# Kernel tuning notes

Measured on AMD Instinct MI355X. Metric: run time of the kernel, lower is better.

Reference implementation:

```python
import jax, jax.numpy as jnp
import numpy as np

B, D, K, BETA = 32, 64, 1024, 0.25


def _conv(x, w, b, s=1, p=0):
    y = jax.lax.conv_general_dilated(x, w, (s, s), [(p, p), (p, p)],
                                     dimension_numbers=('NCHW', 'OIHW', 'NCHW'))
    return y + b[None, :, None, None]


def _tconv(x, w, b):
    # PyTorch ConvTranspose2d(k=4, s=2, p=1); w layout (C_in, C_out, 4, 4)
    wt = jnp.flip(w, (2, 3)).transpose(1, 0, 2, 3)
    y = jax.lax.conv_general_dilated(x, wt, (1, 1), [(2, 2), (2, 2)],
                                     lhs_dilation=(2, 2),
                                     dimension_numbers=('NCHW', 'OIHW', 'NCHW'))
    return y + b[None, :, None, None]


def _res(x, w1, b1, w2, b2):
    # Residual: x + conv1x1(relu(conv3x3(relu(x))))  (no BN config)
    h = _conv(jax.nn.relu(x), w1, b1, 1, 1)
    h = _conv(jax.nn.relu(h), w2, b2, 1, 0)
    return x + h


def setup_inputs() -> dict:
    ks = iter(jax.random.split(jax.random.key(0), 64))

    def w(*shape):
        fan = int(np.prod(shape[1:]))
        return (jax.random.normal(next(ks), shape, jnp.float32) / np.sqrt(fan)).astype(jnp.float32)

    def z(n):
        return jnp.zeros((n,), jnp.float32)

    inp = dict(
        x=jax.random.normal(next(ks), (B, 3, 256, 256), jnp.float32),
        enc_w0=w(64, 3, 4, 4), enc_b0=z(64),
        enc_w1=w(128, 64, 4, 4), enc_b1=z(128),
        enc_w2=w(256, 128, 4, 4), enc_b2=z(256),
        enc_r0_w1=w(64, 256, 3, 3), enc_r0_b1=z(64),
        enc_r0_w2=w(256, 64, 1, 1), enc_r0_b2=z(256),
        enc_r1_w1=w(64, 256, 3, 3), enc_r1_b1=z(64),
        enc_r1_w2=w(256, 64, 1, 1), enc_r1_b2=z(256),
        enc_adj_w=w(D, 256, 1, 1), enc_adj_b=z(D),
        codebook=(jax.random.normal(next(ks), (K, D), jnp.float32) / np.sqrt(D)).astype(jnp.float32),
        dec_adj_w=w(256, D, 1, 1), dec_adj_b=z(256),
        dec_r0_w1=w(64, 256, 3, 3), dec_r0_b1=z(64),
        dec_r0_w2=w(256, 64, 1, 1), dec_r0_b2=z(256),
        dec_r1_w1=w(64, 256, 3, 3), dec_r1_b1=z(64),
        dec_r1_w2=w(256, 64, 1, 1), dec_r1_b2=z(256),
        dec_tw0=w(256, 128, 4, 4), dec_tb0=z(128),
        dec_tw1=w(128, 64, 4, 4), dec_tb1=z(64),
        dec_tw2=w(64, 32, 4, 4), dec_tb2=z(32),
        out_w=w(3, 32, 1, 1), out_b=z(3),
    )
    return inp


def reference(x, enc_w0, enc_b0, enc_w1, enc_b1, enc_w2, enc_b2,
              enc_r0_w1, enc_r0_b1, enc_r0_w2, enc_r0_b2,
              enc_r1_w1, enc_r1_b1, enc_r1_w2, enc_r1_b2,
              enc_adj_w, enc_adj_b, codebook, dec_adj_w, dec_adj_b,
              dec_r0_w1, dec_r0_b1, dec_r0_w2, dec_r0_b2,
              dec_r1_w1, dec_r1_b1, dec_r1_w2, dec_r1_b2,
              dec_tw0, dec_tb0, dec_tw1, dec_tb1, dec_tw2, dec_tb2,
              out_w, out_b):
    # ---------- encoder (M=7: three stride-2 convs, no BN) ----------
    h = jax.nn.relu(_conv(x, enc_w0, enc_b0, 2, 1))   # [B,64,128,128]
    h = jax.nn.relu(_conv(h, enc_w1, enc_b1, 2, 1))   # [B,128,64,64]
    h = jax.nn.relu(_conv(h, enc_w2, enc_b2, 2, 1))   # [B,256,32,32]
    h = _res(h, enc_r0_w1, enc_r0_b1, enc_r0_w2, enc_r0_b2)
    h = _res(h, enc_r1_w1, enc_r1_b1, enc_r1_w2, enc_r1_b2)
    zlat = _conv(h, enc_adj_w, enc_adj_b)             # [B,D,32,32]
    # ---------- vector quantization ----------
    zp = zlat.transpose(0, 2, 3, 1)                   # [B,32,32,D]
    zf = zp.reshape(-1, D)                            # [N,D], N = B*32*32
    d = (jnp.sum(zf * zf, 1, keepdims=True)
         - 2.0 * (zf @ codebook.T)
         + jnp.sum(codebook * codebook, 1)[None, :])  # [N,K]
    idx = jnp.argmin(d, axis=1)                       # [N] codebook indices
    q = codebook[idx].reshape(zp.shape)
    sg = jax.lax.stop_gradient
    e_loss = jnp.mean((sg(q) - zp) ** 2)              # commitment
    q_loss = jnp.mean((q - sg(zp)) ** 2)              # codebook
    vq_loss = q_loss + BETA * e_loss
    q_st = zp + sg(q - zp)                            # straight-through
    counts = jnp.zeros((K,), jnp.float32).at[idx].add(1.0)
    probs = counts / zf.shape[0]
    perplexity = jnp.exp(-jnp.sum(probs * jnp.log(probs + 1e-10)))
    hq = q_st.transpose(0, 3, 1, 2)                   # [B,D,32,32]
    # ---------- decoder (M=7: three stride-2 transposed convs) ----------
    h = _conv(hq, dec_adj_w, dec_adj_b)               # [B,256,32,32]
    h = _res(h, dec_r0_w1, dec_r0_b1, dec_r0_w2, dec_r0_b2)
    h = _res(h, dec_r1_w1, dec_r1_b1, dec_r1_w2, dec_r1_b2)
    h = jax.nn.relu(_tconv(h, dec_tw0, dec_tb0))      # [B,128,64,64]
    h = jax.nn.relu(_tconv(h, dec_tw1, dec_tb1))      # [B,64,128,128]
    h = jax.nn.relu(_tconv(h, dec_tw2, dec_tb2))      # [B,32,256,256]
    x_recon = _conv(h, out_w, out_b)                  # [B,3,256,256]
    return x_recon, vq_loss, perplexity
```

## Files before the change

kernel.cpp:

```cpp
#include <hip/hip_runtime.h>
#include <math.h>

typedef __attribute__((ext_vector_type(4))) float f32x4;
typedef __attribute__((ext_vector_type(8))) short short8;
typedef __attribute__((ext_vector_type(4))) unsigned int u32x4;
typedef unsigned short ushort_t;
typedef unsigned int uint_t;

static const size_t A_OFF      = 0;
static const size_t C_OFF      = 0;
static const size_t D_OFF      = 9469952;
static const size_t E_OFF      = 18939904;
static const size_t Q_OFF      = 21037056;
static const size_t B_OFF      = 34611200;
static const size_t CBT_OFF    = 52453376;
static const size_t CNORM_OFF  = 52518912;
static const size_t COUNTS_OFF = 52519936;
static const size_t SUMSQ_OFF  = 52520960;
static const size_t WT_OFF     = 52520964;

__device__ __forceinline__ ushort_t f2b(float f) {
  uint_t u = __float_as_uint(f);
  uint_t r = (u + 0x7FFFu + ((u >> 16) & 1u)) >> 16;
  return (ushort_t)r;
}
__device__ __forceinline__ float b2f(ushort_t h) {
  return __uint_as_float(((uint_t)h) << 16);
}

__global__ void k_halo(float* __restrict__ buf, int HP, int WP) {
  const int plane = blockIdx.x;
  float* p = buf + (size_t)plane * HP * WP;
  const int ring = 2 * (HP + WP) - 4;
  for (int i = threadIdx.x; i < ring; i += blockDim.x) {
    int idx;
    if (i < WP) idx = i;
    else if (i < 2 * WP) idx = (HP - 1) * WP + (i - WP);
    else {
      const int j = i - 2 * WP;
      const int r = 1 + (j >> 1);
      idx = r * WP + ((j & 1) ? (WP - 1) : 0);
    }
    p[idx] = 0.0f;
  }
}
__global__ void k_zero(float* __restrict__ counts, float* __restrict__ sumsq) {
  const int t = blockIdx.x * 256 + threadIdx.x;
  if (t < 1024) counts[t] = 0.0f;
  if (t == 0) sumsq[0] = 0.0f;
}

__device__ __forceinline__ void wt_conv_body(const float* w, float* wT,
                                             int Cin, int Cout, int K) {
  const int n = Cin * Cout * K;
  for (int i = blockIdx.x * 256 + threadIdx.x; i < n; i += gridDim.x * 256) {
    const int co = i % Cout;
    const int k  = (i / Cout) % K;
    const int ci = i / (Cout * K);
    wT[i] = w[((size_t)co * Cin + ci) * K + k];
  }
}
__global__ void k_wt_conv_multi(const float* w0, float* o0, const float* w1, float* o1,
                                const float* w2, float* o2) {
  if (blockIdx.y == 0) wt_conv_body(w0, o0, 3, 64, 16);
  else if (blockIdx.y == 1) wt_conv_body(w1, o1, 256, 64, 1);
  else wt_conv_body(w2, o2, 64, 256, 1);
}
__device__ __forceinline__ void wtb_body(const float* w, ushort_t* wbT,
                                         int Cin, int Cout) {
  const int n = 4 * Cout * Cin * 4;
  for (int i = blockIdx.x * 256 + threadIdx.x; i < n; i += gridDim.x * 256) {
    const int tap = i & 3;
    const int ci  = (i >> 2) % Cin;
    const int co  = ((i >> 2) / Cin) % Cout;
    const int ph  = (i >> 2) / (Cin * Cout);
    const int ey = ph >> 1, ex = ph & 1;
    const int ty = tap >> 1, tx = tap & 1;
    const int kidx = (3 - 2 * ty - ey) * 4 + (3 - 2 * tx - ex);
    wbT[i] = f2b(w[((size_t)ci * Cout + co) * 16 + kidx]);
  }
}
__global__ void k_wtb_multi(const float* t0, ushort_t* o0, const float* t1, ushort_t* o1,
                            const float* t2, ushort_t* o2) {
  if (blockIdx.y == 0) wtb_body(t0, o0, 256, 128);
  else if (blockIdx.y == 1) wtb_body(t1, o1, 128, 64);
  else wtb_body(t2, o2, 64, 32);
}
__device__ __forceinline__ void wsplit_body(const float* w, ushort_t* wh,
                                            ushort_t* wl, int n) {
  for (int i = blockIdx.x * 256 + threadIdx.x; i < n; i += gridDim.x * 256) {
    const float v = w[i];
    const ushort_t h = f2b(v);
    wh[i] = h;
    wl[i] = f2b(v - b2f(h));
  }
}
__global__ void k_wsplit_enc(const float* w1, ushort_t* h1, ushort_t* l1,
                             const float* w2, ushort_t* h2, ushort_t* l2) {
  if (blockIdx.y == 0) wsplit_body(w1, h1, l1, 131072);
  else wsplit_body(w2, h2, l2, 524288);
}
__global__ void k_wsplit_w2m(const float* a, ushort_t* ah, ushort_t* al,
                             const float* b, ushort_t* bh, ushort_t* bl,
                             const float* c, ushort_t* ch, ushort_t* cl,
                             const float* d, ushort_t* dh, ushort_t* dl) {
  if (blockIdx.y == 0) wsplit_body(a, ah, al, 16384);
  else if (blockIdx.y == 1) wsplit_body(b, bh, bl, 16384);
  else if (blockIdx.y == 2) wsplit_body(c, ch, cl, 16384);
  else wsplit_body(d, dh, dl, 16384);
}
__device__ __forceinline__ void wt3_body(const float* w, ushort_t* wh, ushort_t* wl) {
  const int n = 9 * 64 * 256;
  for (int i = blockIdx.x * 256 + threadIdx.x; i < n; i += gridDim.x * 256) {
    const int ci = i & 255;
    const int co = (i >> 8) & 63;
    const int t  = i >> 14;
    const float v = w[((size_t)co * 256 + ci) * 9 + t];
    const ushort_t h = f2b(v);
    wh[i] = h;
    wl[i] = f2b(v - b2f(h));
  }
}
__global__ void k_wt3split_multi(const float* a, ushort_t* ah, ushort_t* al,
                                 const float* b, ushort_t* bh, ushort_t* bl,
                                 const float* c, ushort_t* ch, ushort_t* cl,
                                 const float* d, ushort_t* dh, ushort_t* dl) {
  if (blockIdx.y == 0) wt3_body(a, ah, al);
  else if (blockIdx.y == 1) wt3_body(b, bh, bl);
  else if (blockIdx.y == 2) wt3_body(c, ch, cl);
  else wt3_body(d, dh, dl);
}
__global__ void k_cbt(const float* __restrict__ cb, float* __restrict__ cbT,
                      float* __restrict__ cnorm) {
  const int c = blockIdx.x * 256 + threadIdx.x;
  float s = 0.0f;
  for (int ci = 0; ci < 64; ++ci) {
    const float v = cb[(size_t)c * 64 + ci];
    s += v * v;
    cbT[(size_t)ci * 1024 + c] = v;
  }
  cnorm[c] = s;
}

__global__ __launch_bounds__(256) void k_conv4s2_s3(
    const float* __restrict__ in, const float* __restrict__ wT,
    const float* __restrict__ bias, float* __restrict__ out) {
  const int b   = blockIdx.z;
  const int co0 = blockIdx.y << 4;
  const int oy0 = (blockIdx.x >> 2) << 5;
  const int ox0 = (blockIdx.x & 3) << 5;
  const int tid = threadIdx.x;
  const int ty = tid >> 4, tx = tid & 15;
  __shared__ float tin[3][66][67];
  float acc[4][16];
#pragma unroll
  for (int p = 0; p < 4; ++p)
#pragma unroll
    for (int co = 0; co < 16; ++co) acc[p][co] = 0.0f;

  const int iy0 = (oy0 << 1) - 1, ix0 = (ox0 << 1) - 1;
  for (int c = 0; c < 3; ++c) {
    const float* ip = in + (size_t)(b * 3 + c) * 65536;
    for (int j = tid; j < 66 * 66; j += 256) {
      const int r = j / 66, col = j - r * 66;
      const int iy = iy0 + r, ix = ix0 + col;
      float v = 0.0f;
      if ((unsigned)iy < 256u && (unsigned)ix < 256u) v = ip[iy * 256 + ix];
      tin[c][r][col] = v;
    }
  }
  __syncthreads();
#pragma unroll
  for (int c = 0; c < 3; ++c) {
    const float* wp = wT + (size_t)c * 16 * 64 + co0;
#pragma unroll
    for (int ky = 0; ky < 4; ++ky)
#pragma unroll
      for (int kx = 0; kx < 4; ++kx) {
        const float v0 = tin[c][2 * ty + ky][2 * tx + kx];
        const float v1 = tin[c][2 * ty + ky][2 * tx + 32 + kx];
        const float v2 = tin[c][2 * ty + 32 + ky][2 * tx + kx];
        const float v3 = tin[c][2 * ty + 32 + ky][2 * tx + 32 + kx];
        const float* wk = wp + (ky * 4 + kx) * 64;
#pragma unroll
        for (int co = 0; co < 16; ++co) {
          const float wv = wk[co];
          acc[0][co] = fmaf(v0, wv, acc[0][co]);
          acc[1][co] = fmaf(v1, wv, acc[1][co]);
          acc[2][co] = fmaf(v2, wv, acc[2][co]);
          acc[3][co] = fmaf(v3, wv, acc[3][co]);
        }
      }
  }
#pragma unroll
  for (int co = 0; co < 16; ++co) {
    const float bv = bias[co0 + co];
    float* op = out + (size_t)(b * 64 + co0 + co) * 16900;
    op[(size_t)(oy0 + ty + 1) * 130 + ox0 + tx + 1]        = fmaxf(acc[0][co] + bv, 0.0f);
    op[(size_t)(oy0 + ty + 1) * 130 + ox0 + tx + 17]       = fmaxf(acc[1][co] + bv, 0.0f);
    op[(size_t)(oy0 + ty + 17) * 130 + ox0 + tx + 1]       = fmaxf(acc[2][co] + bv, 0.0f);
    op[(size_t)(oy0 + ty + 17) * 130 + ox0 + tx + 17]      = fmaxf(acc[3][co] + bv, 0.0f);
  }
}

template <int WSHIFT, int CIN, int COUT, int WP, int INSTRIDE, int WOP, int OUTSTRIDE>
__global__ __launch_bounds__(256) void k_conv4s2_mfma(
    const float* __restrict__ in, const ushort_t* __restrict__ wbh,
    const ushort_t* __restrict__ wbl, const float* __restrict__ bias,
    float* __restrict__ out) {
  constexpr int W = 1 << WSHIFT;
  constexpr int NCH = CIN / 2;
  __shared__ __align__(16) short lsAh[64 * 40];
  __shared__ __align__(16) short lsAl[64 * 40];
  __shared__ __align__(16) short lsBh[64 * 40];
  __shared__ __align__(16) short lsBl[64 * 40];

  const int tid = threadIdx.x;
  const int b = blockIdx.z;
  const int co_b0 = blockIdx.y << 6;
  const int pxb0 = blockIdx.x << 6;

  const int spx = tid & 63;
  const int kg  = tid >> 6;
  const int sy = (pxb0 + spx) >> WSHIFT;
  const int sx = (pxb0 + spx) & (W - 1);
  const float* ipa = in + (size_t)(b * CIN + (kg >> 1)) * INSTRIDE
                   + (size_t)(2 * sy + 2 * (kg & 1)) * WP + 2 * sx;
  const ushort_t* wbase_h = wbh + (size_t)(co_b0 + spx) * (CIN * 16) + kg * 8;
  const ushort_t* wbase_l = wbl + (size_t)(co_b0 + spx) * (CIN * 16) + kg * 8;

  const int lane = tid & 63, wid = tid >> 6;
  const int wm = wid & 1, wn = wid >> 1;
  const int arow = lane & 15, ag = lane >> 4;

  f32x4 acc[2][2];
#pragma unroll
  for (int m = 0; m < 2; ++m)
#pragma unroll
    for (int n = 0; n < 2; ++n) acc[m][n] = (f32x4){0.f, 0.f, 0.f, 0.f};

  float pa[8];
  u32x4 pbh, pbl;
  auto loadch = [&](int ch) {
    const float* p = ipa + (size_t)ch * 2 * INSTRIDE;
    pa[0] = p[0];  pa[1] = p[1];      pa[2] = p[2];      pa[3] = p[3];
    pa[4] = p[WP]; pa[5] = p[WP + 1]; pa[6] = p[WP + 2]; pa[7] = p[WP + 3];
    pbh = *(const u32x4*)(wbase_h + (size_t)ch * 32);
    pbl = *(const u32x4*)(wbase_l + (size_t)ch * 32);
  };

  loadch(0);
  for (int ch = 0; ch < NCH; ++ch) {
    __syncthreads();
    u32x4 vh, vl;
#pragma unroll
    for (int j = 0; j < 4; ++j) {
      const ushort_t h0 = f2b(pa[2 * j]);
      const ushort_t h1 = f2b(pa[2 * j + 1]);
      const ushort_t l0 = f2b(pa[2 * j] - b2f(h0));
      const ushort_t l1 = f2b(pa[2 * j + 1] - b2f(h1));
      vh[j] = (uint_t)h0 | ((uint_t)h1 << 16);
      vl[j] = (uint_t)l0 | ((uint_t)l1 << 16);
    }
    *(u32x4*)(&lsAh[spx * 40 + kg * 8]) = vh;
    *(u32x4*)(&lsAl[spx * 40 + kg * 8]) = vl;
    *(u32x4*)(&lsBh[spx * 40 + kg * 8]) = pbh;
    *(u32x4*)(&lsBl[spx * 40 + kg * 8]) = pbl;
    if (ch + 1 < NCH) loadch(ch + 1);
    __syncthreads();
    short8 ah[2], al[2], bh[2], bl[2];
#pragma unroll
    for (int m = 0; m < 2; ++m) {
      ah[m] = *(const short8*)(&lsAh[(wm * 32 + m * 16 + arow) * 40 + ag * 8]);
      al[m] = *(const short8*)(&lsAl[(wm * 32 + m * 16 + arow) * 40 + ag * 8]);
    }
#pragma unroll
    for (int n = 0; n < 2; ++n) {
      bh[n] = *(const short8*)(&lsBh[(wn * 32 + n * 16 + arow) * 40 + ag * 8]);
      bl[n] = *(const short8*)(&lsBl[(wn * 32 + n * 16 + arow) * 40 + ag * 8]);
    }
#pragma unroll
    for (int m = 0; m < 2; ++m)
#pragma unroll
      for (int n = 0; n < 2; ++n) {
        acc[m][n] = __builtin_amdgcn_mfma_f32_16x16x32_bf16(ah[m], bh[n], acc[m][n], 0, 0, 0);
        acc[m][n] = __builtin_amdgcn_mfma_f32_16x16x32_bf16(ah[m], bl[n], acc[m][n], 0, 0, 0);
        acc[m][n] = __builtin_amdgcn_mfma_f32_16x16x32_bf16(al[m], bh[n], acc[m][n], 0, 0, 0);
      }
  }

#pragma unroll
  for (int m = 0; m < 2; ++m)
#pragma unroll
    for (int n = 0; n < 2; ++n) {
      const int col = co_b0 + wn * 32 + n * 16 + arow;
      const float bv = bias[col];
      float* obase = out + (size_t)(b * COUT + col) * OUTSTRIDE;
#pragma unroll
      for (int r = 0; r < 4; ++r) {
        const int pxl = pxb0 + wm * 32 + m * 16 + ag * 4 + r;
        const int yy = pxl >> WSHIFT, xx = pxl & (W - 1);
        obase[(size_t)(yy + 1) * WOP + (xx + 1)] = fmaxf(acc[m][n][r] + bv, 0.0f);
      }
    }
}

__global__ __launch_bounds__(512) void k_res_mfma(
    const float* __restrict__ in, const ushort_t* __restrict__ w3h,
    const ushort_t* __restrict__ w3l, const float* __restrict__ b1,
    const ushort_t* __restrict__ w2h, const ushort_t* __restrict__ w2l,
    const float* __restrict__ b2, float* __restrict__ out) {
  __shared__ __align__(16) short smem[10240];
  short* lsAh = smem;
  short* lsAl = smem + 2560;
  short* lsBh = smem + 5120;
  short* lsBl = smem + 7680;

  const int tid = threadIdx.x;
  const int b = blockIdx.z;
  const int pxb0 = blockIdx.x << 6;
  const bool isA = tid < 256;
  const int sidx = tid & 63;
  const int skg  = (tid >> 6) & 3;

  const int py = (pxb0 + sidx) >> 5;
  const int pxx = (pxb0 + sidx) & 31;
  const float* ipa = in + (size_t)b * 256 * 1156 + (size_t)py * 34 + pxx;

  const int lane = tid & 63, wid = tid >> 6;
  const int wm = wid & 1, wn = wid >> 1;
  const int arow = lane & 15, ag = lane >> 4;

  f32x4 acc[2];
  acc[0] = (f32x4){0.f, 0.f, 0.f, 0.f};
  acc[1] = (f32x4){0.f, 0.f, 0.f, 0.f};

  float pa[8];
  u32x4 pbh, pbl;
  auto loadit = [&](int it) {
    const int t = it >> 3, ck = it & 7;
    if (isA) {
      const int dy = t / 3, dx = t - 3 * (t / 3);
      const float* p = ipa + (size_t)(ck * 32 + skg * 8) * 1156 + dy * 34 + dx;
#pragma unroll
      for (int j = 0; j < 8; ++j) pa[j] = p[(size_t)j * 1156];
    } else {
      const ushort_t* ph = w3h + ((size_t)(t * 64 + sidx) << 8) + ck * 32 + skg * 8;
      const ushort_t* pl = w3l + ((size_t)(t * 64 + sidx) << 8) + ck * 32 + skg * 8;
      pbh = *(const u32x4*)ph;
      pbl = *(const u32x4*)pl;
    }
  };

  loadit(0);
  for (int it = 0; it < 72; ++it) {
    __syncthreads();
    if (isA) {
      u32x4 vh, vl;
#pragma unroll
      for (int j = 0; j < 4; ++j) {
        const float v0 = fmaxf(pa[2 * j], 0.0f);
        const float v1 = fmaxf(pa[2 * j + 1], 0.0f);
        const ushort_t h0 = f2b(v0);
        const ushort_t h1 = f2b(v1);
        const ushort_t l0 = f2b(v0 - b2f(h0));
        const ushort_t l1 = f2b(v1 - b2f(h1));
        vh[j] = (uint_t)h0 | ((uint_t)h1 << 16);
        vl[j] = (uint_t)l0 | ((uint_t)l1 << 16);
      }
      *(u32x4*)(&lsAh[sidx * 40 + skg * 8]) = vh;
      *(u32x4*)(&lsAl[sidx * 40 + skg * 8]) = vl;
    } else {
      *(u32x4*)(&lsBh[sidx * 40 + skg * 8]) = pbh;
      *(u32x4*)(&lsBl[sidx * 40 + skg * 8]) = pbl;
    }
    if (it + 1 < 72) loadit(it + 1);
    __syncthreads();
    short8 ah[2], al[2];
#pragma unroll
    for (int m = 0; m < 2; ++m) {
      ah[m] = *(const short8*)(&lsAh[(wm * 32 + m * 16 + arow) * 40 + ag * 8]);
      al[m] = *(const short8*)(&lsAl[(wm * 32 + m * 16 + arow) * 40 + ag * 8]);
    }
    const short8 bh = *(const short8*)(&lsBh[(wn * 16 + arow) * 40 + ag * 8]);
    const short8 bl = *(const short8*)(&lsBl[(wn * 16 + arow) * 40 + ag * 8]);
#pragma unroll
    for (int m = 0; m < 2; ++m) {
      acc[m] = __builtin_amdgcn_mfma_f32_16x16x32_bf16(ah[m], bh, acc[m], 0, 0, 0);
      acc[m] = __builtin_amdgcn_mfma_f32_16x16x32_bf16(ah[m], bl, acc[m], 0, 0, 0);
      acc[m] = __builtin_amdgcn_mfma_f32_16x16x32_bf16(al[m], bh, acc[m], 0, 0, 0);
    }
  }

  __syncthreads();
  {
    const float bv = b1[wn * 16 + arow];
    short* hh = smem;
    short* hl = smem + 4608;
#pragma unroll
    for (int m = 0; m < 2; ++m)
#pragma unroll
      for (int r = 0; r < 4; ++r) {
        const int pxl = wm * 32 + m * 16 + ag * 4 + r;
        const float v = fmaxf(acc[m][r] + bv, 0.0f);
        const ushort_t h = f2b(v);
        hh[pxl * 72 + wn * 16 + arow] = (short)h;
        hl[pxl * 72 + wn * 16 + arow] = (short)f2b(v - b2f(h));
      }
  }
  __syncthreads();

  const int m2 = wid & 3;
  const int nh = wid >> 2;
  const short* hh = smem;
  const short* hl = smem + 4608;
  short8 a2h[2], a2l[2];
#pragma unroll
  for (int c = 0; c < 2; ++c) {
    a2h[c] = *(const short8*)(&hh[(m2 * 16 + arow) * 72 + c * 32 + ag * 8]);
    a2l[c] = *(const short8*)(&hl[(m2 * 16 + arow) * 72 + c * 32 + ag * 8]);
  }
  const int px0 = pxb0 + m2 * 16 + ag * 4;
  const int yy0 = px0 >> 5, xx0 = px0 & 31;
  const int ridx = (yy0 + 1) * 34 + xx0 + 1;

  short8 cbh[2], cbl[2], nbh[2], nbl[2];
  float rv[4], nrv[4], bvc, nbvc;
  auto loadj = [&](int j, short8* oh, short8* ol, float* rr, float* bb) {
    const int col2 = (nh * 8 + j) * 16 + arow;
#pragma unroll
    for (int c = 0; c < 2; ++c) {
      oh[c] = *(const short8*)(w2h + (size_t)col2 * 64 + c * 32 + ag * 8);
      ol[c] = *(const short8*)(w2l + (size_t)col2 * 64 + c * 32 + ag * 8);
    }
    const float* rbase = in + (size_t)(b * 256 + col2) * 1156 + ridx;
#pragma unroll
    for (int r = 0; r < 4; ++r) rr[r] = rbase[r];
    *bb = b2[col2];
  };

  loadj(0, cbh, cbl, rv, &bvc);
#pragma unroll
  for (int j = 0; j < 8; ++j) {
    if (j + 1 < 8) loadj(j + 1, nbh, nbl, nrv, &nbvc);
    f32x4 acc2 = (f32x4){0.f, 0.f, 0.f, 0.f};
#pragma unroll
    for (int c = 0; c < 2; ++c) {
      acc2 = __builtin_amdgcn_mfma_f32_16x16x32_bf16(a2h[c], cbh[c], acc2, 0, 0, 0);
      acc2 = __builtin_amdgcn_mfma_f32_16x16x32_bf16(a2h[c], cbl[c], acc2, 0, 0, 0);
      acc2 = __builtin_amdgcn_mfma_f32_16x16x32_bf16(a2l[c], cbh[c], acc2, 0, 0, 0);
    }
    const int col2 = (nh * 8 + j) * 16 + arow;
    float* obase = out + (size_t)(b * 256 + col2) * 1156 + ridx;
#pragma unroll
    for (int r = 0; r < 4; ++r) obase[r] = acc2[r] + bvc + rv[r];
#pragma unroll
    for (int c = 0; c < 2; ++c) { cbh[c] = nbh[c]; cbl[c] = nbl[c]; }
#pragma unroll
    for (int r = 0; r < 4; ++r) rv[r] = nrv[r];
    bvc = nbvc;
  }
}

template <int IN_RELU, int HAS_RES, int IN_PAD, int OUT_PAD>
__global__ __launch_bounds__(256) void k_conv1x1_px(
    const float* __restrict__ in, const float* __restrict__ wT,
    const float* __restrict__ bias, const float* __restrict__ res,
    float* __restrict__ out, int Cin, int Cout) {
  const int b   = blockIdx.z;
  const int co0 = blockIdx.y << 4;
  const int px  = blockIdx.x * 256 + threadIdx.x;
  const int ppad = 35 + px + 2 * (px >> 5);
  const int ioff = IN_PAD ? ppad : px;
  const int istr = IN_PAD ? 1156 : 1024;
  const int ooff = OUT_PAD ? ppad : px;
  const int ostr = OUT_PAD ? 1156 : 1024;
  float acc[16];
#pragma unroll
  for (int co = 0; co < 16; ++co) acc[co] = 0.0f;
  const float* ip = in + (size_t)b * Cin * istr + ioff;
  const float* wp = wT + co0;
  for (int ci = 0; ci < Cin; ++ci) {
    float v = *ip;
    if (IN_RELU) v = fmaxf(v, 0.0f);
    ip += istr;
#pragma unroll
    for (int co = 0; co < 16; ++co) acc[co] = fmaf(v, wp[co], acc[co]);
    wp += Cout;
  }
  float* op = out + (size_t)(b * Cout + co0) * ostr + ooff;
  const float* rp = res + (size_t)(b * Cout + co0) * ostr + ooff;
#pragma unroll
  for (int co = 0; co < 16; ++co) {
    float r = acc[co] + bias[co0 + co];
    if (HAS_RES) r += rp[(size_t)co * ostr];
    op[(size_t)co * ostr] = r;
  }
}

template <int PXB, int COB, int WSHIFT, int CIN, int COUT, int WP,
          int INSTRIDE, int WOP, int OUTSTRIDE, int FINAL, int GRP>
__global__ __launch_bounds__(256) void k_tconv_mfma(
    const float* __restrict__ in, const ushort_t* __restrict__ wbT,
    const float* __restrict__ bias, const float* __restrict__ ow,
    const float* __restrict__ ob, float* __restrict__ out) {
  constexpr int W = 1 << WSHIFT;
  constexpr int NCH = CIN / 8;
  constexpr int NGRP = NCH / GRP;
  constexpr int PXSH = (PXB == 64) ? 6 : 7;
  constexpr int COSH = (COB == 64) ? 6 : 5;
  constexpr int NKG = (PXB * 4) / 256;
  constexpr int KGSTEP = 256 / PXB;
  __shared__ __align__(16) short lsA[GRP][PXB * 40];
  __shared__ __align__(16) short lsB[GRP][COB * 40];
  __shared__ float pxco[FINAL ? PXB : 1][33];

  const int tid = threadIdx.x;
  const int b = blockIdx.z;
  const int phase = blockIdx.y & 3;
  const int ey = phase >> 1, ex = phase & 1;
  const int co_b0 = (blockIdx.y >> 2) * COB;
  const int pxb0 = blockIdx.x * PXB;

  const int spx = tid & (PXB - 1);
  const int kg0 = tid >> PXSH;
  const int sy = (pxb0 + spx) >> WSHIFT;
  const int sx = (pxb0 + spx) & (W - 1);
  const float* ipa = in + (size_t)b * CIN * INSTRIDE + (size_t)(sy + ey) * WP + (sx + ex);
  const int sco = tid & (COB - 1);
  const int skg = tid >> COSH;
  const bool bstage = (tid < COB * 4);
  const ushort_t* wrow = wbT + ((size_t)(phase * COUT + co_b0 + sco) * CIN) * 4;

  const int lane = tid & 63, wid = tid >> 6;
  const int wm = wid % (PXB / 32), wn = wid / (PXB / 32);
  const int arow = lane & 15, ag = lane >> 4;

  f32x4 acc[2][2];
#pragma unroll
  for (int m = 0; m < 2; ++m)
#pragma unroll
    for (int n = 0; n < 2; ++n) acc[m][n] = (f32x4){0.f, 0.f, 0.f, 0.f};

  float pa[GRP][NKG][8];
  u32x4 pb[GRP];
  auto loadgrp = [&](int g) {
#pragma unroll
    for (int c = 0; c < GRP; ++c) {
      const int ch = g * GRP + c;
#pragma unroll
      for (int k = 0; k < NKG; ++k) {
        const float* p = ipa + (size_t)(ch * 8 + (kg0 + k * KGSTEP) * 2) * INSTRIDE;
        const float* q = p + INSTRIDE;
        pa[c][k][0] = p[0]; pa[c][k][1] = p[1]; pa[c][k][2] = p[WP]; pa[c][k][3] = p[WP + 1];
        pa[c][k][4] = q[0]; pa[c][k][5] = q[1]; pa[c][k][6] = q[WP]; pa[c][k][7] = q[WP + 1];
      }
      if (bstage) pb[c] = *(const u32x4*)(wrow + (size_t)ch * 32 + skg * 8);
    }
  };

  loadgrp(0);
  for (int g = 0; g < NGRP; ++g) {
    __syncthreads();
#pragma unroll
    for (int c = 0; c < GRP; ++c) {
#pragma unroll
      for (int k = 0; k < NKG; ++k) {
        u32x4 pk;
        pk[0] = (uint_t)f2b(pa[c][k][0]) | ((uint_t)f2b(pa[c][k][1]) << 16);
        pk[1] = (uint_t)f2b(pa[c][k][2]) | ((uint_t)f2b(pa[c][k][3]) << 16);
        pk[2] = (uint_t)f2b(pa[c][k][4]) | ((uint_t)f2b(pa[c][k][5]) << 16);
        pk[3] = (uint_t)f2b(pa[c][k][6]) | ((uint_t)f2b(pa[c][k][7]) << 16);
        *(u32x4*)(&lsA[c][spx * 40 + (kg0 + k * KGSTEP) * 8]) = pk;
      }
      if (bstage) *(u32x4*)(&lsB[c][sco * 40 + skg * 8]) = pb[c];
    }
    if (g + 1 < NGRP) loadgrp(g + 1);
    __syncthreads();
#pragma unroll
    for (int c = 0; c < GRP; ++c) {
      const short8 a0 = *(const short8*)(&lsA[c][(wm * 32 + arow) * 40 + ag * 8]);
      const short8 a1 = *(const short8*)(&lsA[c][(wm * 32 + 16 + arow) * 40 + ag * 8]);
      const short8 b0 = *(const short8*)(&lsB[c][(wn * 32 + arow) * 40 + ag * 8]);
      const short8 b1 = *(const short8*)(&lsB[c][(wn * 32 + 16 + arow) * 40 + ag * 8]);
      acc[0][0] = __builtin_amdgcn_mfma_f32_16x16x32_bf16(a0, b0, acc[0][0], 0, 0, 0);
      acc[0][1] = __builtin_amdgcn_mfma_f32_16x16x32_bf16(a0, b1, acc[0][1], 0, 0, 0);
      acc[1][0] = __builtin_amdgcn_mfma_f32_16x16x32_bf16(a1, b0, acc[1][0], 0, 0, 0);
      acc[1][1] = __builtin_amdgcn_mfma_f32_16x16x32_bf16(a1, b1, acc[1][1], 0, 0, 0);
    }
  }

  if constexpr (!FINAL) {
#pragma unroll
    for (int m = 0; m < 2; ++m)
#pragma unroll
      for (int n = 0; n < 2; ++n) {
        const int col = co_b0 + wn * 32 + n * 16 + arow;
        const float bv = bias[col];
        float* obase = out + (size_t)(b * COUT + col) * OUTSTRIDE;
#pragma unroll
        for (int r = 0; r < 4; ++r) {
          const int pxl = pxb0 + wm * 32 + m * 16 + ag * 4 + r;
          const int yy = pxl >> WSHIFT, xx = pxl & (W - 1);
          obase[(size_t)(2 * yy + ey + 1) * WOP + (2 * xx + ex + 1)] =
              fmaxf(acc[m][n][r] + bv, 0.0f);
        }
      }
  } else {
#pragma unroll
    for (int m = 0; m < 2; ++m)
#pragma unroll
      for (int n = 0; n < 2; ++n) {
        const int col = wn * 32 + n * 16 + arow;
        const float bv = bias[col];
#pragma unroll
        for (int r = 0; r < 4; ++r) {
          const int pxl = wm * 32 + m * 16 + ag * 4 + r;
          pxco[pxl][col] = fmaxf(acc[m][n][r] + bv, 0.0f);
        }
      }
    __syncthreads();
    if (tid < PXB) {
      const int pxg = pxb0 + tid;
      const int yy = pxg >> WSHIFT, xx = pxg & (W - 1);
      const int oy = 2 * yy + ey, ox = 2 * xx + ex;
      float o0 = ob[0], o1 = ob[1], o2 = ob[2];
#pragma unroll
      for (int co = 0; co < 32; ++co) {
        const float v = pxco[tid][co];
        o0 = fmaf(ow[co], v, o0);
        o1 = fmaf(ow[32 + co], v, o1);
        o2 = fmaf(ow[64 + co], v, o2);
      }
      out[((size_t)(b * 3 + 0) * 256 + oy) * 256 + ox] = o0;
      out[((size_t)(b * 3 + 1) * 256 + oy) * 256 + ox] = o1;
      out[((size_t)(b * 3 + 2) * 256 + oy) * 256 + ox] = o2;
    }
  }
}

__global__ __launch_bounds__(256) void k_vq(
    const float* __restrict__ zlat, const float* __restrict__ cbT,
    const float* __restrict__ cnorm, const float* __restrict__ cb,
    float* __restrict__ q, float* __restrict__ counts, float* __restrict__ sumsq) {
  const int tid = threadIdx.x;
  const int px0 = blockIdx.x << 4;
  const int b   = px0 >> 10;
  const int pl0 = px0 & 1023;
  __shared__ float zT[64][17];
  __shared__ float rd[16][256];
  __shared__ int   ri[16][256];
  for (int j = tid; j < 1024; j += 256) {
    const int ci = j >> 4, p = j & 15;
    zT[ci][p] = zlat[(size_t)(b * 64 + ci) * 1024 + pl0 + p];
  }
  __syncthreads();
  float dot[4][16];
#pragma unroll
  for (int k = 0; k < 4; ++k)
#pragma unroll
    for (int p = 0; p < 16; ++p) dot[k][p] = 0.0f;
  for (int ci = 0; ci < 64; ++ci) {
    float z[16];
#pragma unroll
    for (int p = 0; p < 16; ++p) z[p] = zT[ci][p];
#pragma unroll
    for (int k = 0; k < 4; ++k) {
      const float cv = cbT[(size_t)ci * 1024 + (k << 8) + tid];
#pragma unroll
      for (int p = 0; p < 16; ++p) dot[k][p] = fmaf(cv, z[p], dot[k][p]);
    }
  }
  float bd[16]; int bi[16];
#pragma unroll
  for (int p = 0; p < 16; ++p) { bd[p] = 3.4e38f; bi[p] = 0; }
#pragma unroll
  for (int k = 0; k < 4; ++k) {
    const int c = (k << 8) + tid;
    const float cn = cnorm[c];
#pragma unroll
    for (int p = 0; p < 16; ++p) {
      const float d = cn - 2.0f * dot[k][p];
      if (d < bd[p]) { bd[p] = d; bi[p] = c; }
    }
  }
#pragma unroll
  for (int p = 0; p < 16; ++p) { rd[p][tid] = bd[p]; ri[p][tid] = bi[p]; }
  __syncthreads();
  for (int s = 128; s >= 1; s >>= 1) {
    if (tid < s) {
#pragma unroll
      for (int p = 0; p < 16; ++p) {
        const float d2 = rd[p][tid + s]; const int i2 = ri[p][tid + s];
        const float d1 = rd[p][tid];     const int i1 = ri[p][tid];
        if (d2 < d1 || (d2 == d1 && i2 < i1)) { rd[p][tid] = d2; ri[p][tid] = i2; }
      }
    }
    __syncthreads();
  }
  if (tid < 16) atomicAdd(&counts[ri[tid][0]], 1.0f);
  const int p    = tid >> 4;
  const int best = ri[p][0];
  const int cb0  = (tid & 15) << 2;
  float ss = 0.0f;
  float* qp = q + (size_t)b * 65536 + pl0 + p;
#pragma unroll
  for (int cc = 0; cc < 4; ++cc) {
    const int ci = cb0 + cc;
    const float qv = cb[(size_t)best * 64 + ci];
    const float zv = zT[ci][p];
    const float df = qv - zv;
    ss += df * df;
    qp[(size_t)ci * 1024] = qv;
  }
#pragma unroll
  for (int o = 32; o > 0; o >>= 1) ss += __shfl_down(ss, o);
  if ((tid & 63) == 0) atomicAdd(sumsq, ss);
}

__global__ void k_final(const float* __restrict__ counts, const float* __restrict__ sumsq,
                        float* __restrict__ out2) {
  const int tid = threadIdx.x;
  float h = 0.0f;
  for (int k = tid; k < 1024; k += 256) {
    const float pr = counts[k] * (1.0f / 32768.0f);
    h -= pr * logf(pr + 1e-10f);
  }
#pragma unroll
  for (int o = 32; o > 0; o >>= 1) h += __shfl_down(h, o);
  __shared__ float hs[4];
  if ((tid & 63) == 0) hs[tid >> 6] = h;
  __syncthreads();
  if (tid == 0) {
    out2[0] = 1.25f * sumsq[0] * (1.0f / 2097152.0f);
    out2[1] = expf(hs[0] + hs[1] + hs[2] + hs[3]);
  }
}

extern "C" void kernel_launch(void* const* d_in, const int* in_sizes, int n_in,
                              void* d_out, int out_size, void* d_ws, size_t ws_size,
                              hipStream_t stream) {
  const float* x        = (const float*)d_in[0];
  const float* enc_w0   = (const float*)d_in[1];
  const float* enc_b0   = (const float*)d_in[2];
  const float* enc_w1   = (const float*)d_in[3];
  const float* enc_b1   = (const float*)d_in[4];
  const float* enc_w2   = (const float*)d_in[5];
  const float* enc_b2   = (const float*)d_in[6];
  const float* er0w1    = (const float*)d_in[7];
  const float* er0b1    = (const float*)d_in[8];
  const float* er0w2    = (const float*)d_in[9];
  const float* er0b2    = (const float*)d_in[10];
  const float* er1w1    = (const float*)d_in[11];
  const float* er1b1    = (const float*)d_in[12];
  const float* er1w2    = (const float*)d_in[13];
  const float* er1b2    = (const float*)d_in[14];
  const float* eadj_w   = (const float*)d_in[15];
  const float* eadj_b   = (const float*)d_in[16];
  const float* codebook = (const float*)d_in[17];
  const float* dadj_w   = (const float*)d_in[18];
  const float* dadj_b   = (const float*)d_in[19];
  const float* dr0w1    = (const float*)d_in[20];
  const float* dr0b1    = (const float*)d_in[21];
  const float* dr0w2    = (const float*)d_in[22];
  const float* dr0b2    = (const float*)d_in[23];
  const float* dr1w1    = (const float*)d_in[24];
  const float* dr1b1    = (const float*)d_in[25];
  const float* dr1w2    = (const float*)d_in[26];
  const float* dr1b2    = (const float*)d_in[27];
  const float* tw0      = (const float*)d_in[28];
  const float* tb0      = (const float*)d_in[29];
  const float* tw1      = (const float*)d_in[30];
  const float* tb1      = (const float*)d_in[31];
  const float* tw2      = (const float*)d_in[32];
  const float* tb2      = (const float*)d_in[33];
  const float* out_w    = (const float*)d_in[34];
  const float* out_b    = (const float*)d_in[35];

  float* ws = (float*)d_ws;
  float* A      = ws + A_OFF;
  float* Bb     = ws + B_OFF;
  float* C      = ws + C_OFF;
  float* Dq     = ws + D_OFF;
  float* E      = ws + E_OFF;
  float* Q      = ws + Q_OFF;
  float* cbT    = ws + CBT_OFF;
  float* cnorm  = ws + CNORM_OFF;
  float* counts = ws + COUNTS_OFF;
  float* sumsq  = ws + SUMSQ_OFF;

  size_t o = WT_OFF;
  float* wt_enc0  = ws + o; o += (size_t)3 * 16 * 64;
  float* wt_eadj  = ws + o; o += (size_t)256 * 64;
  float* wt_dadj  = ws + o; o += (size_t)64 * 256;
  ushort_t* wbT0 = (ushort_t*)(ws + o); o += 262144;
  ushort_t* wbT1 = (ushort_t*)(ws + o); o += 65536;
  ushort_t* wbT2 = (ushort_t*)(ws + o); o += 16384;
  ushort_t* wsh1 = (ushort_t*)(ws + o); o += 65536;
  ushort_t* wsl1 = (ushort_t*)(ws + o); o += 65536;
  ushort_t* wsh2 = (ushort_t*)(ws + o); o += 262144;
  ushort_t* wsl2 = (ushort_t*)(ws + o); o += 262144;
  ushort_t* w3h_er0 = (ushort_t*)(ws + o); o += 73728;
  ushort_t* w3l_er0 = (ushort_t*)(ws + o); o += 73728;
  ushort_t* w3h_er1 = (ushort_t*)(ws + o); o += 73728;
  ushort_t* w3l_er1 = (ushort_t*)(ws + o); o += 73728;
  ushort_t* w3h_dr0 = (ushort_t*)(ws + o); o += 73728;
  ushort_t* w3l_dr0 = (ushort_t*)(ws + o); o += 73728;
  ushort_t* w3h_dr1 = (ushort_t*)(ws + o); o += 73728;
  ushort_t* w3l_dr1 = (ushort_t*)(ws + o); o += 73728;
  ushort_t* w2h_er0 = (ushort_t*)(ws + o); o += 8192;
  ushort_t* w2l_er0 = (ushort_t*)(ws + o); o += 8192;
  ushort_t* w2h_er1 = (ushort_t*)(ws + o); o += 8192;
  ushort_t* w2l_er1 = (ushort_t*)(ws + o); o += 8192;
  ushort_t* w2h_dr0 = (ushort_t*)(ws + o); o += 8192;
  ushort_t* w2l_dr0 = (ushort_t*)(ws + o); o += 8192;
  ushort_t* w2h_dr1 = (ushort_t*)(ws + o); o += 8192;
  ushort_t* w2l_dr1 = (ushort_t*)(ws + o); o += 8192;

  float* fout = (float*)d_out;

  #define GB(n) (((n) + 255) / 256)
  k_zero<<<4, 256, 0, stream>>>(counts, sumsq);
  k_halo<<<2048, 64, 0, stream>>>(A, 130, 130);
  k_halo<<<4096, 64, 0, stream>>>(Bb, 66, 66);

  k_wt_conv_multi<<<dim3(64, 3), 256, 0, stream>>>(enc_w0, wt_enc0, eadj_w, wt_eadj,
                                                   dadj_w, wt_dadj);
  k_wtb_multi<<<dim3(2048, 3), 256, 0, stream>>>(tw0, wbT0, tw1, wbT1, tw2, wbT2);
  k_wsplit_enc<<<dim3(2048, 2), 256, 0, stream>>>(enc_w1, wsh1, wsl1, enc_w2, wsh2, wsl2);
  k_wsplit_w2m<<<dim3(64, 4), 256, 0, stream>>>(er0w2, w2h_er0, w2l_er0,
                                                er1w2, w2h_er1, w2l_er1,
                                                dr0w2, w2h_dr0, w2l_dr0,
                                                dr1w2, w2h_dr1, w2l_dr1);
  k_wt3split_multi<<<dim3(576, 4), 256, 0, stream>>>(er0w1, w3h_er0, w3l_er0,
                                                     er1w1, w3h_er1, w3l_er1,
                                                     dr0w1, w3h_dr0, w3l_dr0,
                                                     dr1w1, w3h_dr1, w3l_dr1);
  k_cbt<<<4, 256, 0, stream>>>(codebook, cbT, cnorm);

  k_conv4s2_s3<<<dim3(16, 4, 32), 256, 0, stream>>>(x, wt_enc0, enc_b0, A);
  k_conv4s2_mfma<6, 64, 128, 130, 16900, 66, 4356>
      <<<dim3(64, 2, 32), 256, 0, stream>>>(A, wsh1, wsl1, enc_b1, Bb);
  k_halo<<<8192, 64, 0, stream>>>(C, 34, 34);
  k_halo<<<8192, 64, 0, stream>>>(Dq, 34, 34);
  k_conv4s2_mfma<5, 128, 256, 66, 4356, 34, 1156>
      <<<dim3(16, 4, 32), 256, 0, stream>>>(Bb, wsh2, wsl2, enc_b2, C);
  k_res_mfma<<<dim3(16, 1, 32), 512, 0, stream>>>(C, w3h_er0, w3l_er0, er0b1,
                                                  w2h_er0, w2l_er0, er0b2, Dq);
  k_res_mfma<<<dim3(16, 1, 32), 512, 0, stream>>>(Dq, w3h_er1, w3l_er1, er1b1,
                                                  w2h_er1, w2l_er1, er1b2, C);
  k_conv1x1_px<0, 0, 1, 0><<<dim3(4, 4, 32), 256, 0, stream>>>(C, wt_eadj, eadj_b, nullptr, E, 256, 64);
  k_vq<<<2048, 256, 0, stream>>>(E, cbT, cnorm, codebook, Q, counts, sumsq);
  k_conv1x1_px<0, 0, 0, 1><<<dim3(4, 16, 32), 256, 0, stream>>>(Q, wt_dadj, dadj_b, nullptr, C, 64, 256);
  k_res_mfma<<<dim3(16, 1, 32), 512, 0, stream>>>(C, w3h_dr0, w3l_dr0, dr0b1,
                                                  w2h_dr0, w2l_dr0, dr0b2, Dq);
  k_res_mfma<<<dim3(16, 1, 32), 512, 0, stream>>>(Dq, w3h_dr1, w3l_dr1, dr1b1,
                                                  w2h_dr1, w2l_dr1, dr1b2, C);
  k_tconv_mfma<64, 64, 5, 256, 128, 34, 1156, 66, 4356, 0, 2>
      <<<dim3(16, 8, 32), 256, 0, stream>>>(C, wbT0, tb0, nullptr, nullptr, Bb);
  k_halo<<<2048, 64, 0, stream>>>(A, 130, 130);
  k_tconv_mfma<64, 64, 6, 128, 64, 66, 4356, 130, 16900, 0, 2>
      <<<dim3(64, 4, 32), 256, 0, stream>>>(Bb, wbT1, tb1, nullptr, nullptr, A);
  k_tconv_mfma<128, 32, 7, 64, 32, 130, 16900, 0, 0, 1, 1>
      <<<dim3(128, 4, 32), 256, 0, stream>>>(A, wbT2, tb2, out_w, out_b, fout);
  k_final<<<1, 256, 0, stream>>>(counts, sumsq, fout + 6291456);
  #undef GB
}
```

Baseline: 1.669 ms.

## Store decoder intermediate activations as bf16 to halve memory traffic

The last decoder residual block and the first two transposed convs now write their activations as bf16 instead of fp32. The tconv kernels read bf16 directly and pack pairs without per-element conversion. This roughly halves the bytes written and read between decoder stages, which are large at 64x64 and 128x128 resolution, and drops the f32-to-bf16 rounding from the load path. The activations were already rounded to bf16 before the MFMA, so numerics should stay essentially unchanged. New halo-zeroing kernels handle the 16-bit buffers, which alias the existing workspace regions.

Result: no change. 1.639 ms (-1.8%).

```diff
diff --git a/kernel.cpp b/kernel.cpp
--- a/kernel.cpp
+++ b/kernel.cpp
@@ -26,6 +26,9 @@
 }
 __device__ __forceinline__ float b2f(ushort_t h) {
   return __uint_as_float(((uint_t)h) << 16);
+}
+__device__ __forceinline__ uint_t pk2(ushort_t a, ushort_t c) {
+  return (uint_t)a | ((uint_t)c << 16);
 }
 
 __global__ void k_halo(float* __restrict__ buf, int HP, int WP) {
@@ -44,6 +47,22 @@
     p[idx] = 0.0f;
   }
 }
+__global__ void k_halo_h(ushort_t* __restrict__ buf, int HP, int WP) {
+  const int plane = blockIdx.x;
+  ushort_t* p = buf + (size_t)plane * HP * WP;
+  const int ring = 2 * (HP + WP) - 4;
+  for (int i = threadIdx.x; i < ring; i += blockDim.x) {
+    int idx;
+    if (i < WP) idx = i;
+    else if (i < 2 * WP) idx = (HP - 1) * WP + (i - WP);
+    else {
+      const int j = i - 2 * WP;
+      const int r = 1 + (j >> 1);
+      idx = r * WP + ((j & 1) ? (WP - 1) : 0);
+    }
+    p[idx] = (ushort_t)0;
+  }
+}
 __global__ void k_zero(float* __restrict__ counts, float* __restrict__ sumsq) {
   const int t = blockIdx.x * 256 + threadIdx.x;
   if (t < 1024) counts[t] = 0.0f;
@@ -305,6 +324,7 @@
     }
 }
 
+template <int OUTB>
 __global__ __launch_bounds__(512) void k_res_mfma(
     const float* __restrict__ in, const ushort_t* __restrict__ w3h,
     const ushort_t* __restrict__ w3l, const float* __restrict__ b1,
@@ -451,9 +471,15 @@
       acc2 = __builtin_amdgcn_mfma_f32_16x16x32_bf16(a2l[c], cbh[c], acc2, 0, 0, 0);
     }
     const int col2 = (nh * 8 + j) * 16 + arow;
-    float* obase = out + (size_t)(b * 256 + col2) * 1156 + ridx;
-#pragma unroll
-    for (int r = 0; r < 4; ++r) obase[r] = acc2[r] + bvc + rv[r];
+    if constexpr (OUTB) {
+      ushort_t* ob16 = (ushort_t*)out + (size_t)(b * 256 + col2) * 1156 + ridx;
+#pragma unroll
+      for (int r = 0; r < 4; ++r) ob16[r] = f2b(acc2[r] + bvc + rv[r]);
+    } else {
+      float* obase = out + (size_t)(b * 256 + col2) * 1156 + ridx;
+#pragma unroll
+      for (int r = 0; r < 4; ++r) obase[r] = acc2[r] + bvc + rv[r];
+    }
 #pragma unroll
     for (int c = 0; c < 2; ++c) { cbh[c] = nbh[c]; cbl[c] = nbl[c]; }
 #pragma unroll
@@ -499,11 +525,11 @@
 }
 
 template <int PXB, int COB, int WSHIFT, int CIN, int COUT, int WP,
-          int INSTRIDE, int WOP, int OUTSTRIDE, int FINAL, int GRP>
+          int INSTRIDE, int WOP, int OUTSTRIDE, int FINAL, int GRP, int INB, int OUTB>
 __global__ __launch_bounds__(256) void k_tconv_mfma(
-    const float* __restrict__ in, const ushort_t* __restrict__ wbT,
+    const void* __restrict__ in_, const ushort_t* __restrict__ wbT,
     const float* __restrict__ bias, const float* __restrict__ ow,
-    const float* __restrict__ ob, float* __restrict__ out) {
+    const float* __restrict__ ob, void* __restrict__ out_) {
   constexpr int W = 1 << WSHIFT;
   constexpr int NCH = CIN / 8;
   constexpr int NGRP = NCH / GRP;
@@ -526,7 +552,7 @@
   const int kg0 = tid >> PXSH;
   const int sy = (pxb0 + spx) >> WSHIFT;
   const int sx = (pxb0 + spx) & (W - 1);
-  const float* ipa = in + (size_t)b * CIN * INSTRIDE + (size_t)(sy + ey) * WP + (sx + ex);
+  const size_t abase = (size_t)b * CIN * INSTRIDE + (size_t)(sy + ey) * WP + (sx + ex);
   const int sco = tid & (COB - 1);
   const int skg = tid >> COSH;
   const bool bstage = (tid < COB * 4);
@@ -543,6 +569,7 @@
     for (int n = 0; n < 2; ++n) acc[m][n] = (f32x4){0.f, 0.f, 0.f, 0.f};
 
   float pa[GRP][NKG][8];
+  uint_t pu[GRP][NKG][4];
   u32x4 pb[GRP];
   auto loadgrp = [&](int g) {
 #pragma unroll
@@ -550,10 +577,20 @@
       const int ch = g * GRP + c;
 #pragma unroll
       for (int k = 0; k < NKG; ++k) {
-        const float* p = ipa + (size_t)(ch * 8 + (kg0 + k * KGSTEP) * 2) * INSTRIDE;
-        const float* q = p + INSTRIDE;
-        pa[c][k][0] = p[0]; pa[c][k][1] = p[1]; pa[c][k][2] = p[WP]; pa[c][k][3] = p[WP + 1];
-        pa[c][k][4] = q[0]; pa[c][k][5] = q[1]; pa[c][k][6] = q[WP]; pa[c][k][7] = q[WP + 1];
+        const size_t off = abase + (size_t)(ch * 8 + (kg0 + k * KGSTEP) * 2) * INSTRIDE;
+        if constexpr (INB) {
+          const ushort_t* p = (const ushort_t*)in_ + off;
+          const ushort_t* q = p + INSTRIDE;
+          pu[c][k][0] = pk2(p[0], p[1]);
+          pu[c][k][1] = pk2(p[WP], p[WP + 1]);
+          pu[c][k][2] = pk2(q[0], q[1]);
+          pu[c][k][3] = pk2(q[WP], q[WP + 1]);
+        } else {
+          const float* p = (const float*)in_ + off;
+          const float* q = p + INSTRIDE;
+          pa[c][k][0] = p[0]; pa[c][k][1] = p[1]; pa[c][k][2] = p[WP]; pa[c][k][3] = p[WP + 1];
+          pa[c][k][4] = q[0]; pa[c][k][5] = q[1]; pa[c][k][6] = q[WP]; pa[c][k][7] = q[WP + 1];
+        }
       }
       if (bstage) pb[c] = *(const u32x4*)(wrow + (size_t)ch * 32 + skg * 8);
     }
@@ -567,10 +604,15 @@
 #pragma unroll
       for (int k = 0; k < NKG; ++k) {
         u32x4 pk;
-        pk[0] = (uint_t)f2b(pa[c][k][0]) | ((uint_t)f2b(pa[c][k][1]) << 16);
-        pk[1] = (uint_t)f2b(pa[c][k][2]) | ((uint_t)f2b(pa[c][k][3]) << 16);
-        pk[2] = (uint_t)f2b(pa[c][k][4]) | ((uint_t)f2b(pa[c][k][5]) << 16);
-        pk[3] = (uint_t)f2b(pa[c][k][6]) | ((uint_t)f2b(pa[c][k][7]) << 16);
+        if constexpr (INB) {
+          pk[0] = pu[c][k][0]; pk[1] = pu[c][k][1];
+          pk[2] = pu[c][k][2]; pk[3] = pu[c][k][3];
+        } else {
+          pk[0] = (uint_t)f2b(pa[c][k][0]) | ((uint_t)f2b(pa[c][k][1]) << 16);
+          pk[1] = (uint_t)f2b(pa[c][k][2]) | ((uint_t)f2b(pa[c][k][3]) << 16);
+          pk[2] = (uint_t)f2b(pa[c][k][4]) | ((uint_t)f2b(pa[c][k][5]) << 16);
+          pk[3] = (uint_t)f2b(pa[c][k][6]) | ((uint_t)f2b(pa[c][k][7]) << 16);
+        }
         *(u32x4*)(&lsA[c][spx * 40 + (kg0 + k * KGSTEP) * 8]) = pk;
       }
       if (bstage) *(u32x4*)(&lsB[c][sco * 40 + skg * 8]) = pb[c];
@@ -597,13 +639,15 @@
       for (int n = 0; n < 2; ++n) {
         const int col = co_b0 + wn * 32 + n * 16 + arow;
         const float bv = bias[col];
-        float* obase = out + (size_t)(b * COUT + col) * OUTSTRIDE;
 #pragma unroll
         for (int r = 0; r < 4; ++r) {
           const int pxl = pxb0 + wm * 32 + m * 16 + ag * 4 + r;
           const int yy = pxl >> WSHIFT, xx = pxl & (W - 1);
-          obase[(size_t)(2 * yy + ey + 1) * WOP + (2 * xx + ex + 1)] =
-              fmaxf(acc[m][n][r] + bv, 0.0f);
+          const size_t oidx = (size_t)(b * COUT + col) * OUTSTRIDE
+                            + (size_t)(2 * yy + ey + 1) * WOP + (2 * xx + ex + 1);
+          const float v = fmaxf(acc[m][n][r] + bv, 0.0f);
+          if constexpr (OUTB) ((ushort_t*)out_)[oidx] = f2b(v);
+          else ((float*)out_)[oidx] = v;
         }
       }
   } else {
@@ -632,9 +676,10 @@
         o1 = fmaf(ow[32 + co], v, o1);
         o2 = fmaf(ow[64 + co], v, o2);
       }
-      out[((size_t)(b * 3 + 0) * 256 + oy) * 256 + ox] = o0;
-      out[((size_t)(b * 3 + 1) * 256 + oy) * 256 + ox] = o1;
-      out[((size_t)(b * 3 + 2) * 256 + oy) * 256 + ox] = o2;
+      float* outf = (float*)out_;
+      outf[((size_t)(b * 3 + 0) * 256 + oy) * 256 + ox] = o0;
+      outf[((size_t)(b * 3 + 1) * 256 + oy) * 256 + ox] = o1;
+      outf[((size_t)(b * 3 + 2) * 256 + oy) * 256 + ox] = o2;
     }
   }
 }
@@ -788,6 +833,9 @@
   float* cnorm  = ws + CNORM_OFF;
   float* counts = ws + COUNTS_OFF;
   float* sumsq  = ws + SUMSQ_OFF;
+  ushort_t* Cb16  = (ushort_t*)ws;
+  ushort_t* Bb16u = (ushort_t*)(ws + B_OFF);
+  ushort_t* A16u  = (ushort_t*)ws;
 
   size_t o = WT_OFF;
   float* wt_enc0  = ws + o; o += (size_t)3 * 16 * 64;
@@ -819,7 +867,6 @@
 
   float* fout = (float*)d_out;
 
-  #define GB(n) (((n) + 255) / 256)
   k_zero<<<4, 256, 0, stream>>>(counts, sumsq);
   k_halo<<<2048, 64, 0, stream>>>(A, 130, 130);
   k_halo<<<4096, 64, 0, stream>>>(Bb, 66, 66);
@@ -845,24 +892,25 @@
   k_halo<<<8192, 64, 0, stream>>>(Dq, 34, 34);
   k_conv4s2_mfma<5, 128, 256, 66, 4356, 34, 1156>
       <<<dim3(16, 4, 32), 256, 0, stream>>>(Bb, wsh2, wsl2, enc_b2, C);
-  k_res_mfma<<<dim3(16, 1, 32), 512, 0, stream>>>(C, w3h_er0, w3l_er0, er0b1,
-                                                  w2h_er0, w2l_er0, er0b2, Dq);
-  k_res_mfma<<<dim3(16, 1, 32), 512, 0, stream>>>(Dq, w3h_er1, w3l_er1, er1b1,
-                                                  w2h_er1, w2l_er1, er1b2, C);
+  k_halo_h<<<4096, 64, 0, stream>>>(Bb16u, 66, 66);
+  k_res_mfma<0><<<dim3(16, 1, 32), 512, 0, stream>>>(C, w3h_er0, w3l_er0, er0b1,
+                                                     w2h_er0, w2l_er0, er0b2, Dq);
+  k_res_mfma<0><<<dim3(16, 1, 32), 512, 0, stream>>>(Dq, w3h_er1, w3l_er1, er1b1,
+                                                     w2h_er1, w2l_er1, er1b2, C);
   k_conv1x1_px<0, 0, 1, 0><<<dim3(4, 4, 32), 256, 0, stream>>>(C, wt_eadj, eadj_b, nullptr, E, 256, 64);
   k_vq<<<2048, 256, 0, stream>>>(E, cbT, cnorm, codebook, Q, counts, sumsq);
   k_conv1x1_px<0, 0, 0, 1><<<dim3(4, 16, 32), 256, 0, stream>>>(Q, wt_dadj, dadj_b, nullptr, C, 64, 256);
-  k_res_mfma<<<dim3(16, 1, 32), 512, 0, stream>>>(C, w3h_dr0, w3l_dr0, dr0b1,
-                                                  w2h_dr0, w2l_dr0, dr0b2, Dq);
-  k_res_mfma<<<dim3(16, 1, 32), 512, 0, stream>>>(Dq, w3h_dr1, w3l_dr1, dr1b1,
-                                                  w2h_dr1, w2l_dr1, dr1b2, C);
-  k_tconv_mfma<64, 64, 5, 256, 128, 34, 1156, 66, 4356, 0, 2>
-      <<<dim3(16, 8, 32), 256, 0, stream>>>(C, wbT0, tb0, nullptr, nullptr, Bb);
-  k_halo<<<2048, 64, 0, stream>>>(A, 130, 130);
-  k_tconv_mfma<64, 64, 6, 128, 64, 66, 4356, 130, 16900, 0, 2>
-      <<<dim3(64, 4, 32), 256, 0, stream>>>(Bb, wbT1, tb1, nullptr, nullptr, A);
-  k_tconv_mfma<128, 32, 7, 64, 32, 130, 16900, 0, 0, 1, 1>
-      <<<dim3(128, 4, 32), 256, 0, stream>>>(A, wbT2, tb2, out_w, out_b, fout);
+  k_res_mfma<0><<<dim3(16, 1, 32), 512, 0, stream>>>(C, w3h_dr0, w3l_dr0, dr0b1,
+                                                     w2h_dr0, w2l_dr0, dr0b2, Dq);
+  k_halo_h<<<8192, 64, 0, stream>>>(Cb16, 34, 34);
+  k_res_mfma<1><<<dim3(16, 1, 32), 512, 0, stream>>>(Dq, w3h_dr1, w3l_dr1, dr1b1,
+                                                     w2h_dr1, w2l_dr1, dr1b2, (float*)Cb16);
+  k_tconv_mfma<64, 64, 5, 256, 128, 34, 1156, 66, 4356, 0, 2, 1, 1>
+      <<<dim3(16, 8, 32), 256, 0, stream>>>(Cb16, wbT0, tb0, nullptr, nullptr, Bb16u);
+  k_halo_h<<<2048, 64, 0, stream>>>(A16u, 130, 130);
+  k_tconv_mfma<64, 64, 6, 128, 64, 66, 4356, 130, 16900, 0, 2, 1, 1>
+      <<<dim3(64, 4, 32), 256, 0, stream>>>(Bb16u, wbT1, tb1, nullptr, nullptr, A16u);
+  k_tconv_mfma<128, 32, 7, 64, 32, 130, 16900, 0, 0, 1, 1, 1, 0>
+      <<<dim3(128, 4, 32), 256, 0, stream>>>(A16u, wbT2, tb2, out_w, out_b, fout);
   k_final<<<1, 256, 0, stream>>>(counts, sumsq, fout + 6291456);
-  #undef GB
-}
+}
```
